# Kernel optimization log

Measured on AMD Instinct MI355X. Metric: run time of the kernel, lower is better.

The kernel has to match this reference:

```python
import jax, jax.numpy as jnp
import numpy as np

DT_MIN, DT_MAX = 0.001, 0.1
CHUNK = 64


def setup_inputs() -> dict:
    key = jax.random.key(0)
    ks = jax.random.split(key, 8)
    b, L, D = 2, 4096, 1024
    d_inner, d_state, nheads, K = 2048, 128, 32, 4
    conv_dim = d_inner + 2 * d_state            # 2304
    d_in_proj = 2 * d_inner + 2 * d_state + nheads  # 4384
    f32 = jnp.float32
    return {
        'x': jax.random.normal(ks[0], (b, L, D), f32),
        'in_proj_w': jax.random.normal(ks[1], (d_in_proj, D), f32) * (D ** -0.5),
        'conv_w': jax.random.normal(ks[2], (conv_dim, K), f32) * 0.3,
        'conv_b': jnp.zeros((conv_dim,), f32),
        'dt_bias': jax.random.normal(ks[3], (nheads,), f32) * 0.5,
        'A_log': jnp.log(jax.random.uniform(ks[4], (nheads,), f32, 1.0, 16.0)),
        'D_skip': jnp.ones((nheads,), f32),
        'norm_w': jnp.ones((d_inner,), f32),
        'out_proj_w': jax.random.normal(ks[5], (D, d_inner), f32) * (d_inner ** -0.5),
        'ln_w': jnp.ones((D,), f32),
        'ln_b': jnp.zeros((D,), f32),
    }


def reference(x, in_proj_w, conv_w, conv_b, dt_bias, A_log, D_skip, norm_w, out_proj_w, ln_w, ln_b):
    b, L, d_model = x.shape
    d_inner = norm_w.shape[0]
    nheads = A_log.shape[0]
    hd = d_inner // nheads                      # headdim = 64
    conv_dim = conv_w.shape[0]
    d_state = (conv_dim - d_inner) // 2
    Q = CHUNK
    c = L // Q

    # ---- Mamba2 in_proj ----
    zxbcdt = jnp.einsum('bld,kd->blk', x, in_proj_w)
    z = zxbcdt[..., :d_inner]                                   # gate
    xBC = zxbcdt[..., d_inner:d_inner + conv_dim]
    dt_raw = zxbcdt[..., d_inner + conv_dim:]                   # (b,L,h)

    # ---- causal depthwise conv1d (kernel 4) + SiLU ----
    K = conv_w.shape[1]
    xp = jnp.pad(xBC, ((0, 0), (K - 1, 0), (0, 0)))
    conv = sum(xp[:, k:k + L, :] * conv_w[:, k] for k in range(K)) + conv_b
    xBC = jax.nn.silu(conv)
    x_ssm = xBC[..., :d_inner]
    Bm = xBC[..., d_inner:d_inner + d_state]                    # (b,L,n)
    Cm = xBC[..., d_inner + d_state:]                           # (b,L,n)

    # ---- bounded dt (sigmoid, per SSMBlock fix) ----
    dt = DT_MIN + (DT_MAX - DT_MIN) * jax.nn.sigmoid(dt_raw + dt_bias)  # (b,L,h)
    A = -jnp.exp(A_log)                                          # (h,)

    # ---- chunked SSD selective scan ----
    xh = x_ssm.reshape(b, c, Q, nheads, hd)
    dtc = dt.reshape(b, c, Q, nheads)
    x_dt = xh * dtc[..., None]
    dA = jnp.einsum('bcqh,h->bhcq', dtc, A)
    Acum = jnp.cumsum(dA, axis=-1)                               # (b,h,c,Q)
    Bc = Bm.reshape(b, c, Q, d_state)
    Cc = Cm.reshape(b, c, Q, d_state)

    # intra-chunk (diagonal blocks)
    seg = Acum[..., :, None] - Acum[..., None, :]                # (b,h,c,Q,Q)
    mask = jnp.tril(jnp.ones((Q, Q), bool))
    Lmat = jnp.exp(jnp.where(mask, seg, -jnp.inf))
    Yd = jnp.einsum('bcqn,bcsn,bhcqs,bcshp->bcqhp', Cc, Bc, Lmat, x_dt)

    # chunk end-states
    decay_states = jnp.exp(Acum[..., -1:] - Acum)                # (b,h,c,Q)
    states = jnp.einsum('bcqn,bhcq,bcqhp->bchpn', Bc, decay_states, x_dt)
    chunk_decay = jnp.exp(Acum[..., -1])                         # (b,h,c)

    def step(carry, inp):
        st, dec = inp
        return dec[..., None, None] * carry + st, carry

    _, prevs = jax.lax.scan(
        step, jnp.zeros((b, nheads, hd, d_state), x.dtype),
        (jnp.moveaxis(states, 1, 0), jnp.moveaxis(chunk_decay, 2, 0)))
    prevs = jnp.moveaxis(prevs, 0, 1)                            # (b,c,h,p,n)

    # inter-chunk contribution
    Yo = jnp.einsum('bcqn,bchpn,bhcq->bcqhp', Cc, prevs, jnp.exp(Acum))

    Y = (Yd + Yo).reshape(b, L, nheads, hd) + D_skip[None, None, :, None] * xh.reshape(b, L, nheads, hd)
    y = Y.reshape(b, L, d_inner)

    # ---- gated RMSNorm + out_proj ----
    y = y * jax.nn.silu(z)
    y = y * jax.lax.rsqrt(jnp.mean(y * y, axis=-1, keepdims=True) + 1e-5) * norm_w
    out = jnp.einsum('bli,di->bld', y, out_proj_w)

    # ---- SSMBlock: LayerNorm + (eval-mode dropout) + residual ----
    mu = jnp.mean(out, axis=-1, keepdims=True)
    var = jnp.mean((out - mu) ** 2, axis=-1, keepdims=True)
    ln = (out - mu) * jax.lax.rsqrt(var + 1e-5) * ln_w + ln_b
    return x + ln
```

## Files before the change

kernel.cpp:

```cpp
#include <hip/hip_runtime.h>
#include <math.h>

#define BSZ     2
#define LEN     4096
#define DMODEL  1024
#define DINNER  2048
#define DSTATE  128
#define NHEADS  32
#define HDIM    64
#define CONVDIM 2304
#define QC      64
#define NCHUNK  64
#define ROWS    (BSZ*LEN)
#define SDIM    (HDIM*DSTATE)
#define PB      136
#define PT      72
#define CGRP    (CONVDIM/8)

typedef __attribute__((ext_vector_type(8))) short short8;
typedef __attribute__((ext_vector_type(4))) float f32x4;

__device__ __forceinline__ float silu_(float x){ return x / (1.0f + expf(-x)); }
__device__ __forceinline__ float sigm_(float x){ return 1.0f / (1.0f + expf(-x)); }
__device__ __forceinline__ float bf2f(unsigned short u){
    return __uint_as_float(((unsigned int)u) << 16);
}
__device__ __forceinline__ unsigned short f2bf(float f){
    unsigned int u = __float_as_uint(f);
    u = (u + 0x7fffu + ((u >> 16) & 1u)) >> 16;
    return (unsigned short)u;
}

__device__ __forceinline__ int swzcol(int row, int col) {
    return ((((col >> 3) ^ (row >> 3)) & 7) << 3) | (col & 7);
}
__device__ __forceinline__ int swzblk(int row, int blk) {
    return (((blk ^ (row >> 3)) & 7) << 3);
}

__device__ __forceinline__ void gload16(const void* g, void* l) {
    __builtin_amdgcn_global_load_lds(
        (const __attribute__((address_space(1))) unsigned int*)g,
        (__attribute__((address_space(3))) unsigned int*)l, 16, 0, 0);
}

__device__ __forceinline__ void cast4(const float* __restrict__ src,
                                      unsigned short* __restrict__ dst, int i) {
    const float4 v = *(const float4*)(src + (size_t)i * 4);
    ushort4 o;
    o.x = f2bf(v.x); o.y = f2bf(v.y); o.z = f2bf(v.z); o.w = f2bf(v.w);
    *(ushort4*)(dst + (size_t)i * 4) = o;
}

__global__ __launch_bounds__(256) void cast3(const float* __restrict__ s0, unsigned short* __restrict__ d0, int n0,
                                             const float* __restrict__ s1, unsigned short* __restrict__ d1, int n1,
                                             const float* __restrict__ s2, unsigned short* __restrict__ d2, int n2) {
    int i = blockIdx.x * 256 + threadIdx.x;
    if (i < n0) { cast4(s0, d0, i); return; }
    i -= n0;
    if (i < n1) { cast4(s1, d1, i); return; }
    i -= n1;
    if (i < n2) cast4(s2, d2, i);
}

__device__ __forceinline__ void stage_half(const unsigned short* __restrict__ G,
                                           void* ldsbase, int w, int lane,
                                           size_t rowbase, int lda, int kcol) {
#pragma unroll
    for (int u = 0; u < 2; u++) {
        const int f = w * 128 + u * 64 + lane;
        const int r = f >> 3;
        const int cl = (lane & 7) ^ (lane >> 3);
        gload16(G + rowbase + (size_t)r * lda + kcol + cl * 8,
                (char*)ldsbase + f * 16);
    }
}

#define WAITV(n) asm volatile("s_waitcnt vmcnt(" #n ")" ::: "memory")
#define LGKM0    asm volatile("s_waitcnt lgkmcnt(0)" ::: "memory")
#define BARRIER  do { asm volatile("" ::: "memory"); \
                      __builtin_amdgcn_s_barrier();  \
                      asm volatile("" ::: "memory"); } while (0)

#define READ_A(dst, buf, half)                                                \
    _Pragma("unroll")                                                         \
    for (int fr = 0; fr < 4; fr++) {                                          \
        const int r_ = (w & 1) * 64 + fr * 16 + l16;                          \
        _Pragma("unroll")                                                     \
        for (int s = 0; s < 2; s++)                                           \
            dst[fr][s] = *(const short8*)((const char*)&lds[buf][0][half][0]  \
                + r_ * 128 + (((s * 4 + quad) ^ rx7) << 4));                  \
    }
#define READ_B(dst, buf, half)                                                \
    _Pragma("unroll")                                                         \
    for (int fc = 0; fc < 2; fc++) {                                          \
        const int r_ = (w >> 1) * 32 + fc * 16 + l16;                         \
        _Pragma("unroll")                                                     \
        for (int s = 0; s < 2; s++)                                           \
            dst[fc][s] = *(const short8*)((const char*)&lds[buf][1][half][0]  \
                + r_ * 128 + (((s * 4 + quad) ^ rx7) << 4));                  \
    }
#define MFMA16(g, af, bfv)                                                    \
    __builtin_amdgcn_s_setprio(1);                                            \
    _Pragma("unroll")                                                         \
    for (int s = 0; s < 2; s++)                                               \
        _Pragma("unroll")                                                     \
        for (int fr = 0; fr < 4; fr++)                                        \
            _Pragma("unroll")                                                 \
            for (int fc = 0; fc < 2; fc++)                                    \
                acc[g][fr][fc] = __builtin_amdgcn_mfma_f32_16x16x32_bf16(     \
                    af[fr][s], bfv[fc][s], acc[g][fr][fc], 0, 0, 0);          \
    __builtin_amdgcn_s_setprio(0);

template<bool BF16OUT>
__global__ __launch_bounds__(512, 2) void gemm8p(const unsigned short* __restrict__ A,
                                                 const unsigned short* __restrict__ B,
                                                 void* __restrict__ C0,
                                                 void* __restrict__ C1,
                                                 int N, int Kfull, int Ks,
                                                 int gx, int nwg1) {
    __shared__ unsigned short lds[2][2][2][8192];
    const int tid = threadIdx.x;
    const int w = tid >> 6, lane = tid & 63;
    const int quad = lane >> 4, l16 = lane & 15;
    const int rx7 = l16 & 7;

    const int nwg = gridDim.x;
    const int id = blockIdx.x;
    const int q8 = nwg >> 3, r8 = nwg & 7;
    const int xcd = id & 7, idx = id >> 3;
    const int wg = (xcd < r8 ? xcd * (q8 + 1) : r8 * (q8 + 1) + (xcd - r8) * q8) + idx;
    const int sid = wg / nwg1;
    const int wgl = wg % nwg1;
    const int m0 = (wgl / gx) * 256, n0 = (wgl % gx) * 256;
    const int kbase = sid * Ks;
    void* Cout = sid ? C1 : C0;

    const size_t a0r = (size_t)m0 * Kfull;
    const size_t a1r = (size_t)(m0 + 128) * Kfull;
    const size_t b0r = (size_t)n0 * Kfull;
    const size_t b1r = (size_t)(n0 + 128) * Kfull;

    f32x4 acc[4][4][2];
#pragma unroll
    for (int g = 0; g < 4; g++)
#pragma unroll
        for (int i = 0; i < 4; i++)
#pragma unroll
            for (int j = 0; j < 2; j++) acc[g][i][j] = (f32x4){0.f, 0.f, 0.f, 0.f};

    const int NT = Ks >> 6;
    stage_half(A, &lds[0][0][0][0], w, lane, a0r, Kfull, kbase);
    stage_half(B, &lds[0][1][0][0], w, lane, b0r, Kfull, kbase);
    stage_half(A, &lds[0][0][1][0], w, lane, a1r, Kfull, kbase);
    stage_half(B, &lds[0][1][1][0], w, lane, b1r, Kfull, kbase);
    stage_half(A, &lds[1][0][0][0], w, lane, a0r, Kfull, kbase + 64);
    stage_half(B, &lds[1][1][0][0], w, lane, b0r, Kfull, kbase + 64);
    stage_half(A, &lds[1][0][1][0], w, lane, a1r, Kfull, kbase + 64);
    WAITV(6); BARRIER;

    short8 af0[4][2], af1[4][2], bf0[2][2], bf1[2][2];
    for (int p = 0; p < (NT >> 1) - 1; p++) {
        const int kb1 = kbase + (2 * p + 1) * 64;
        const int ka2 = kbase + (2 * p + 2) * 64;
        const int kb2 = kbase + (2 * p + 3) * 64;
        READ_A(af0, 0, 0); READ_B(bf0, 0, 0);
        stage_half(B, &lds[1][1][1][0], w, lane, b1r, Kfull, kb1);
        BARRIER; MFMA16(0, af0, bf0); LGKM0; BARRIER;
        READ_A(af1, 0, 1);
        stage_half(A, &lds[0][0][0][0], w, lane, a0r, Kfull, ka2);
        BARRIER; MFMA16(1, af1, bf0); LGKM0; BARRIER;
        READ_B(bf1, 0, 1);
        stage_half(B, &lds[0][1][0][0], w, lane, b0r, Kfull, ka2);
        BARRIER; MFMA16(2, af0, bf1); LGKM0; BARRIER;
        stage_half(A, &lds[0][0][1][0], w, lane, a1r, Kfull, ka2);
        WAITV(6); BARRIER; MFMA16(3, af1, bf1); LGKM0; BARRIER;
        READ_A(af0, 1, 0); READ_B(bf0, 1, 0);
        stage_half(B, &lds[0][1][1][0], w, lane, b1r, Kfull, ka2);
        BARRIER; MFMA16(0, af0, bf0); LGKM0; BARRIER;
        READ_A(af1, 1, 1);
        stage_half(A, &lds[1][0][0][0], w, lane, a0r, Kfull, kb2);
        BARRIER; MFMA16(1, af1, bf0); LGKM0; BARRIER;
        READ_B(bf1, 1, 1);
        stage_half(B, &lds[1][1][0][0], w, lane, b0r, Kfull, kb2);
        BARRIER; MFMA16(2, af0, bf1); LGKM0; BARRIER;
        stage_half(A, &lds[1][0][1][0], w, lane, a1r, Kfull, kb2);
        WAITV(6); BARRIER; MFMA16(3, af1, bf1); LGKM0; BARRIER;
    }
    READ_A(af0, 0, 0); READ_B(bf0, 0, 0);
    stage_half(B, &lds[1][1][1][0], w, lane, b1r, Kfull, kbase + (NT - 1) * 64);
    MFMA16(0, af0, bf0);
    READ_A(af1, 0, 1);
    MFMA16(1, af1, bf0);
    READ_B(bf1, 0, 1);
    MFMA16(2, af0, bf1);
    MFMA16(3, af1, bf1);
    WAITV(0); LGKM0; BARRIER;
    READ_A(af0, 1, 0); READ_B(bf0, 1, 0);
    MFMA16(0, af0, bf0);
    READ_A(af1, 1, 1);
    MFMA16(1, af1, bf0);
    READ_B(bf1, 1, 1);
    MFMA16(2, af0, bf1);
    MFMA16(3, af1, bf1);

#pragma unroll
    for (int g = 0; g < 4; g++) {
        const int qm = g & 1, qn = g >> 1;
        const int mb = m0 + qm * 128 + (w & 1) * 64;
        const int nb2 = n0 + qn * 128 + (w >> 1) * 32;
#pragma unroll
        for (int fr = 0; fr < 4; fr++)
#pragma unroll
            for (int fc = 0; fc < 2; fc++) {
                const int n = nb2 + fc * 16 + l16;
#pragma unroll
                for (int rr = 0; rr < 4; rr++) {
                    const int m = mb + fr * 16 + quad * 4 + rr;
                    if (BF16OUT)
                        ((unsigned short*)Cout)[(size_t)m * N + n] = f2bf(acc[g][fr][fc][rr]);
                    else
                        ((float*)Cout)[(size_t)m * N + n] = acc[g][fr][fc][rr];
                }
            }
    }
}

__global__ __launch_bounds__(256) void dtproj_mfma(const unsigned short* __restrict__ A,
                                                   const unsigned short* __restrict__ W,
                                                   const float* __restrict__ bias,
                                                   float* __restrict__ dtb,
                                                   int K) {
    __shared__ unsigned short As[4][2][32 * 32];
    __shared__ unsigned short Ws[4][2][32 * 32];
    __shared__ float red[4][32][32];
    const int tid = threadIdx.x;
    const int w = tid >> 6, lane = tid & 63;
    const int quad = lane >> 4, l16 = lane & 15;
    const int m0 = blockIdx.x * 32;
    const int kbeg = w * (1024 / 4);

    f32x4 acc[2][2];
#pragma unroll
    for (int i = 0; i < 2; i++)
#pragma unroll
        for (int j = 0; j < 2; j++) acc[i][j] = (f32x4){0.f, 0.f, 0.f, 0.f};

#define DTSTAGE(buf, kt)                                                      \
    _Pragma("unroll")                                                         \
    for (int u = 0; u < 2; u++) {                                             \
        const int f = u * 64 + lane;                                          \
        const int row = f >> 2, ke = (f & 3) * 8;                             \
        gload16(A + (size_t)(m0 + row) * K + (kt) + ke,                       \
                (char*)&As[w][buf][0] + f * 16);                              \
        gload16(W + (size_t)row * K + (kt) + ke,                              \
                (char*)&Ws[w][buf][0] + f * 16);                              \
    }

    DTSTAGE(0, kbeg);
    int buf = 0;
    for (int it = 0; it < 8; it++) {
        if (it < 7) { DTSTAGE(buf ^ 1, kbeg + (it + 1) * 32); WAITV(4); }
        else        { WAITV(0); }
        short8 af[2], bfr[2];
#pragma unroll
        for (int i = 0; i < 2; i++)
            af[i] = *(const short8*)((const char*)&As[w][buf][0] + (i * 16 + l16) * 64 + quad * 16);
#pragma unroll
        for (int j = 0; j < 2; j++)
            bfr[j] = *(const short8*)((const char*)&Ws[w][buf][0] + (j * 16 + l16) * 64 + quad * 16);
#pragma unroll
        for (int i = 0; i < 2; i++)
#pragma unroll
            for (int j = 0; j < 2; j++)
                acc[i][j] = __builtin_amdgcn_mfma_f32_16x16x32_bf16(
                    af[i], bfr[j], acc[i][j], 0, 0, 0);
        buf ^= 1;
    }
#pragma unroll
    for (int i = 0; i < 2; i++)
#pragma unroll
        for (int j = 0; j < 2; j++)
#pragma unroll
            for (int r = 0; r < 4; r++)
                red[w][i * 16 + quad * 4 + r][j * 16 + l16] = acc[i][j][r];
    __syncthreads();
#pragma unroll
    for (int e = 0; e < 4; e++) {
        const int o = tid + e * 256;
        const int m = o >> 5, hh = o & 31;
        const float v = red[0][m][hh] + red[1][m][hh] + red[2][m][hh] + red[3][m][hh];
        dtb[(size_t)m0 * NHEADS + o] = 0.001f + 0.099f * sigm_(v + bias[hh]);
    }
}

__global__ __launch_bounds__(256) void conv_silu_w(const unsigned short* __restrict__ xbc,
                                                   const float* __restrict__ cw,
                                                   const float* __restrict__ cb,
                                                   unsigned short* __restrict__ xssm,
                                                   unsigned short* __restrict__ Bb,
                                                   unsigned short* __restrict__ Cb) {
    const int idx = blockIdx.x * 256 + threadIdx.x;
    const int g = idx % CGRP;
    const int rowblk = idx / CGRP;
    const long row0 = (long)rowblk * 4;
    const int lbase = (int)(row0 & (LEN - 1));
    const int j0 = g * 8;

    float4 wv[8];
    float cbv[8];
#pragma unroll
    for (int e = 0; e < 8; e++) {
        wv[e] = *(const float4*)(cw + (size_t)(j0 + e) * 4);
        cbv[e] = cb[j0 + e];
    }

    short8 win[4];
    const short8 zero8 = (short8){0, 0, 0, 0, 0, 0, 0, 0};
#pragma unroll
    for (int t = 0; t < 3; t++) {
        const int lr = lbase - 3 + t;
        win[t] = (lr >= 0) ? *(const short8*)(xbc + (row0 - 3 + t) * CONVDIM + j0)
                           : zero8;
    }
#pragma unroll
    for (int i = 0; i < 4; i++) {
        win[3] = *(const short8*)(xbc + (row0 + i) * CONVDIM + j0);
        short8 o;
#pragma unroll
        for (int e = 0; e < 8; e++) {
            float acc = cbv[e];
            acc += bf2f((unsigned short)win[0][e]) * wv[e].x;
            acc += bf2f((unsigned short)win[1][e]) * wv[e].y;
            acc += bf2f((unsigned short)win[2][e]) * wv[e].z;
            acc += bf2f((unsigned short)win[3][e]) * wv[e].w;
            o[e] = (short)f2bf(silu_(acc));
        }
        const long row = row0 + i;
        if (j0 < DINNER)
            *(short8*)(xssm + row * DINNER + j0) = o;
        else if (j0 < DINNER + DSTATE)
            *(short8*)(Bb + row * DSTATE + (j0 - DINNER)) = o;
        else
            *(short8*)(Cb + row * DSTATE + (j0 - DINNER - DSTATE)) = o;
        win[0] = win[1]; win[1] = win[2]; win[2] = win[3];
    }
}

__global__ __launch_bounds__(64) void acum_kernel(const float* __restrict__ dtb,
                                                  const float* __restrict__ A_log,
                                                  float* __restrict__ Acum) {
    const int c = blockIdx.x, h = blockIdx.y, b = blockIdx.z;
    const int q = threadIdx.x;
    const float Av = -expf(A_log[h]);
    float v = dtb[((size_t)b * LEN + c * QC + q) * NHEADS + h] * Av;
#pragma unroll
    for (int off = 1; off < 64; off <<= 1) {
        const float n = __shfl_up(v, off, 64);
        if (q >= off) v += n;
    }
    Acum[(((size_t)b * NHEADS + h) * NCHUNK + c) * QC + q] = v;
}

__global__ __launch_bounds__(256) void chunk_mfma(const unsigned short* __restrict__ xssm,
                                                  const unsigned short* __restrict__ Bb,
                                                  const unsigned short* __restrict__ Cb,
                                                  const float* __restrict__ dtb,
                                                  const float* __restrict__ Acum,
                                                  const float* __restrict__ Dskip,
                                                  unsigned short* __restrict__ Y,
                                                  unsigned short* __restrict__ states) {
    const int c = blockIdx.x, h = blockIdx.y, b = blockIdx.z;
    const int tid = threadIdx.x;
    const int wave = tid >> 6, lane = tid & 63;
    const int quad = lane >> 4, l16 = lane & 15;

    __shared__ __attribute__((aligned(16))) unsigned short Bsh[8704];
    __shared__ __attribute__((aligned(16))) unsigned short Csh[9216];
    __shared__ __attribute__((aligned(16))) unsigned short xTs[4608];
    __shared__ float ac[QC], dts[QC], decs[QC];

    const size_t rowbase = (size_t)b * LEN + c * QC;
    if (tid < QC) {
        ac[tid]  = Acum[(((size_t)b * NHEADS + h) * NCHUNK + c) * QC + tid];
        dts[tid] = dtb[(rowbase + tid) * NHEADS + h];
    }
#pragma unroll
    for (int u = 0; u < 4; u++) {
        const int vi = u * 256 + tid;
        const int s = vi >> 4, n0 = (vi & 15) * 8;
        *(short8*)&Bsh[s * PB + n0] = *(const short8*)(Bb + (rowbase + s) * DSTATE + n0);
        *(short8*)&Csh[s * PB + n0] = *(const short8*)(Cb + (rowbase + s) * DSTATE + n0);
    }
#pragma unroll
    for (int u = 0; u < 2; u++) {
        const int vi = u * 256 + tid;
        const int q = vi >> 3, p0 = (vi & 7) * 8;
        const short8 v = *(const short8*)(xssm + (rowbase + q) * DINNER + h * HDIM + p0);
#pragma unroll
        for (int j = 0; j < 8; j++) {
            const int p = p0 + j;
            xTs[p * PT + swzcol(p, q)] = (unsigned short)v[j];
        }
    }
    __syncthreads();
    if (tid < QC) decs[tid] = expf(ac[QC - 1] - ac[tid]) * dts[tid];

    f32x4 S[4];
#pragma unroll
    for (int j = 0; j < 4; j++) S[j] = (f32x4){0.f, 0.f, 0.f, 0.f};
    const int qa = wave * 16 + l16;
#pragma unroll
    for (int ks = 0; ks < 4; ks++) {
        const short8 a = *(const short8*)&Csh[qa * PB + ks * 32 + quad * 8];
#pragma unroll
        for (int j = 0; j < 4; j++) {
            const short8 bb = *(const short8*)&Bsh[(j * 16 + l16) * PB + ks * 32 + quad * 8];
            S[j] = __builtin_amdgcn_mfma_f32_16x16x32_bf16(a, bb, S[j], 0, 0, 0);
        }
    }
    unsigned short slv[4][4];
#pragma unroll
    for (int j = 0; j < 4; j++)
#pragma unroll
        for (int r = 0; r < 4; r++) {
            const int q = wave * 16 + quad * 4 + r, s = j * 16 + l16;
            const float v = (s <= q) ? S[j][r] * expf(ac[q] - ac[s]) * dts[s] : 0.f;
            slv[j][r] = f2bf(v);
        }
    __syncthreads();

    {
        const int sin = lane & 7;
        const int ng  = lane >> 3;
#pragma unroll
        for (int so = 0; so < 2; so++) {
            const int s = (wave * 2 + so) * 8 + sin;
            const float d = decs[s];
            const int cbk = s >> 3;
#pragma unroll
            for (int nh = 0; nh < 2; nh++) {
                const int noct = ng + 8 * nh;
                const int colphys = (((cbk ^ noct) & 7) << 3) | (s & 7);
#pragma unroll
                for (int j = 0; j < 8; j++) {
                    const int n = noct * 8 + ((j + sin) & 7);
                    Csh[n * PT + colphys] = f2bf(bf2f(Bsh[s * PB + n]) * d);
                }
            }
        }
    }
    __syncthreads();

#pragma unroll
    for (int j = 0; j < 4; j++)
#pragma unroll
        for (int r = 0; r < 4; r++) {
            const int row = wave * 16 + quad * 4 + r;
            const int col = j * 16 + l16;
            Bsh[row * PT + swzcol(row, col)] = slv[j][r];
        }
    __syncthreads();

    f32x4 yd[4];
#pragma unroll
    for (int j = 0; j < 4; j++) yd[j] = (f32x4){0.f, 0.f, 0.f, 0.f};
#pragma unroll
    for (int ks = 0; ks < 2; ks++) {
        const int blk = ks * 4 + quad;
        const short8 a = *(const short8*)&Bsh[qa * PT + swzblk(qa, blk)];
#pragma unroll
        for (int j = 0; j < 4; j++) {
            const int row = j * 16 + l16;
            const short8 xb = *(const short8*)&xTs[row * PT + swzblk(row, blk)];
            yd[j] = __builtin_amdgcn_mfma_f32_16x16x32_bf16(a, xb, yd[j], 0, 0, 0);
        }
    }
    const float Dh = Dskip[h];
#pragma unroll
    for (int j = 0; j < 4; j++)
#pragma unroll
        for (int r = 0; r < 4; r++) {
            const int q = wave * 16 + quad * 4 + r, p = j * 16 + l16;
            const float v = yd[j][r] + Dh * bf2f(xTs[p * PT + swzcol(p, q)]);
            Y[(rowbase + q) * DINNER + h * HDIM + p] = f2bf(v);
        }

    f32x4 st[8];
#pragma unroll
    for (int j = 0; j < 8; j++) st[j] = (f32x4){0.f, 0.f, 0.f, 0.f};
#pragma unroll
    for (int ks = 0; ks < 2; ks++) {
        const int blk = ks * 4 + quad;
        const short8 a = *(const short8*)&xTs[qa * PT + swzblk(qa, blk)];
#pragma unroll
        for (int j = 0; j < 8; j++) {
            const int row = j * 16 + l16;
            const short8 bb = *(const short8*)&Csh[row * PT + swzblk(row, blk)];
            st[j] = __builtin_amdgcn_mfma_f32_16x16x32_bf16(a, bb, st[j], 0, 0, 0);
        }
    }
    const size_t sbase = (((size_t)b * NHEADS + h) * NCHUNK + c) * SDIM;
#pragma unroll
    for (int j = 0; j < 8; j++)
#pragma unroll
        for (int r = 0; r < 4; r++) {
            const int p = wave * 16 + quad * 4 + r, n = j * 16 + l16;
            states[sbase + (size_t)p * DSTATE + n] = f2bf(st[j][r]);
        }
}

__global__ __launch_bounds__(256) void scan_kernel(unsigned short* __restrict__ states,
                                                   const float* __restrict__ Acum) {
    __shared__ float dec[NCHUNK];
    const int bh = blockIdx.y;
    const int pn = blockIdx.x * 256 + threadIdx.x;
    if (threadIdx.x < NCHUNK)
        dec[threadIdx.x] = expf(Acum[((size_t)bh * NCHUNK + threadIdx.x) * QC + (QC - 1)]);
    __syncthreads();
    float carry = 0.f;
    const size_t base = (size_t)bh * NCHUNK * SDIM + pn;
    for (int c = 0; c < NCHUNK; c++) {
        const size_t idx = base + (size_t)c * SDIM;
        const float s = bf2f(states[idx]);
        states[idx] = f2bf(carry);
        carry = dec[c] * carry + s;
    }
}

__global__ __launch_bounds__(256) void yo_mfma(const unsigned short* __restrict__ Cb,
                                               const unsigned short* __restrict__ prevs,
                                               const float* __restrict__ Acum,
                                               unsigned short* __restrict__ Y) {
    const int c = blockIdx.x, h = blockIdx.y, b = blockIdx.z;
    const int tid = threadIdx.x;
    const int wave = tid >> 6, lane = tid & 63;
    const int quad = lane >> 4, l16 = lane & 15;
    __shared__ __attribute__((aligned(16))) unsigned short Csh[8704];
    __shared__ __attribute__((aligned(16))) unsigned short Psh[8704];
    __shared__ float eq[QC];
    const size_t rowbase = (size_t)b * LEN + c * QC;
    const size_t pbase = (((size_t)b * NHEADS + h) * NCHUNK + c) * SDIM;
    if (tid < QC)
        eq[tid] = expf(Acum[(((size_t)b * NHEADS + h) * NCHUNK + c) * QC + tid]);
#pragma unroll
    for (int u = 0; u < 4; u++) {
        const int vi = u * 256 + tid;
        const int r = vi >> 4, n0 = (vi & 15) * 8;
        *(short8*)&Csh[r * PB + n0] = *(const short8*)(Cb + (rowbase + r) * DSTATE + n0);
        *(short8*)&Psh[r * PB + n0] = *(const short8*)(prevs + pbase + (size_t)r * DSTATE + n0);
    }
    __syncthreads();

    f32x4 acc[4];
#pragma unroll
    for (int j = 0; j < 4; j++) acc[j] = (f32x4){0.f, 0.f, 0.f, 0.f};
    const int qa = wave * 16 + l16;
#pragma unroll
    for (int ks = 0; ks < 4; ks++) {
        const short8 a = *(const short8*)&Csh[qa * PB + ks * 32 + quad * 8];
#pragma unroll
        for (int j = 0; j < 4; j++) {
            const short8 bb = *(const short8*)&Psh[(j * 16 + l16) * PB + ks * 32 + quad * 8];
            acc[j] = __builtin_amdgcn_mfma_f32_16x16x32_bf16(a, bb, acc[j], 0, 0, 0);
        }
    }
#pragma unroll
    for (int j = 0; j < 4; j++)
#pragma unroll
        for (int r = 0; r < 4; r++) {
            const int q = wave * 16 + quad * 4 + r, p = j * 16 + l16;
            const size_t off = (rowbase + q) * DINNER + h * HDIM + p;
            Y[off] = f2bf(bf2f(Y[off]) + eq[q] * acc[j][r]);
        }
}

__global__ __launch_bounds__(256) void gate_rms(const unsigned short* __restrict__ Y,
                                                const unsigned short* __restrict__ zbf,
                                                const float* __restrict__ nw,
                                                unsigned short* __restrict__ ybf) {
    const int r = blockIdx.x, tid = threadIdx.x;
    float4 yv[2];
    float ss = 0.f;
#pragma unroll
    for (int u = 0; u < 2; u++) {
        const int col = u * 1024 + tid * 4;
        const ushort4 y4 = *(const ushort4*)(Y + (size_t)r * DINNER + col);
        const ushort4 z4 = *(const ushort4*)(zbf + (size_t)r * DINNER + col);
        float4 y;
        y.x = bf2f(y4.x) * silu_(bf2f(z4.x)); y.y = bf2f(y4.y) * silu_(bf2f(z4.y));
        y.z = bf2f(y4.z) * silu_(bf2f(z4.z)); y.w = bf2f(y4.w) * silu_(bf2f(z4.w));
        yv[u] = y;
        ss += y.x * y.x + y.y * y.y + y.z * y.z + y.w * y.w;
    }
#pragma unroll
    for (int off = 32; off; off >>= 1) ss += __shfl_xor(ss, off, 64);
    __shared__ float red[4];
    if ((tid & 63) == 0) red[tid >> 6] = ss;
    __syncthreads();
    ss = red[0] + red[1] + red[2] + red[3];
    const float scale = rsqrtf(ss / (float)DINNER + 1e-5f);
#pragma unroll
    for (int u = 0; u < 2; u++) {
        const int col = u * 1024 + tid * 4;
        const float4 w4 = *(const float4*)(nw + col);
        ushort4 o;
        o.x = f2bf(yv[u].x * scale * w4.x); o.y = f2bf(yv[u].y * scale * w4.y);
        o.z = f2bf(yv[u].z * scale * w4.z); o.w = f2bf(yv[u].w * scale * w4.w);
        *(ushort4*)(ybf + (size_t)r * DINNER + col) = o;
    }
}

__global__ __launch_bounds__(256) void ln_res(const float* __restrict__ outb,
                                              const float* __restrict__ part,
                                              const float* __restrict__ x,
                                              const float* __restrict__ lw,
                                              const float* __restrict__ lb,
                                              float* __restrict__ out) {
    const int r = blockIdx.x, tid = threadIdx.x;
    const int col = tid * 4;
    float4 v = *(const float4*)(outb + (size_t)r * DMODEL + col);
    const float4 pv = *(const float4*)(part + (size_t)r * DMODEL + col);
    v.x += pv.x; v.y += pv.y; v.z += pv.z; v.w += pv.w;
    float s = v.x + v.y + v.z + v.w;
    float s2 = v.x * v.x + v.y * v.y + v.z * v.z + v.w * v.w;
#pragma unroll
    for (int off = 32; off; off >>= 1) {
        s += __shfl_xor(s, off, 64);
        s2 += __shfl_xor(s2, off, 64);
    }
    __shared__ float rs[4], rs2[4];
    if ((tid & 63) == 0) { rs[tid >> 6] = s; rs2[tid >> 6] = s2; }
    __syncthreads();
    s = rs[0] + rs[1] + rs[2] + rs[3];
    s2 = rs2[0] + rs2[1] + rs2[2] + rs2[3];
    const float mu = s / (float)DMODEL;
    const float var = s2 / (float)DMODEL - mu * mu;
    const float inv = rsqrtf(var + 1e-5f);
    const float4 xw = *(const float4*)(x + (size_t)r * DMODEL + col);
    const float4 w4 = *(const float4*)(lw + col);
    const float4 b4 = *(const float4*)(lb + col);
    float4 o;
    o.x = xw.x + (v.x - mu) * inv * w4.x + b4.x;
    o.y = xw.y + (v.y - mu) * inv * w4.y + b4.y;
    o.z = xw.z + (v.z - mu) * inv * w4.z + b4.z;
    o.w = xw.w + (v.w - mu) * inv * w4.w + b4.w;
    *(float4*)(out + (size_t)r * DMODEL + col) = o;
}

extern "C" void kernel_launch(void* const* d_in, const int* in_sizes, int n_in,
                              void* d_out, int out_size, void* d_ws, size_t ws_size,
                              hipStream_t stream) {
    const float* x          = (const float*)d_in[0];
    const float* in_proj_w  = (const float*)d_in[1];
    const float* conv_w     = (const float*)d_in[2];
    const float* conv_b     = (const float*)d_in[3];
    const float* dt_bias    = (const float*)d_in[4];
    const float* A_log      = (const float*)d_in[5];
    const float* D_skip     = (const float*)d_in[6];
    const float* norm_w     = (const float*)d_in[7];
    const float* out_proj_w = (const float*)d_in[8];
    const float* ln_w       = (const float*)d_in[9];
    const float* ln_b       = (const float*)d_in[10];
    float* out = (float*)d_out;
    float* ws = (float*)d_ws;

    size_t off = 0;
    unsigned short* zbf     = (unsigned short*)(ws + off); off += (size_t)ROWS * DINNER / 2;
    unsigned short* xssm_bf = (unsigned short*)(ws + off); off += (size_t)ROWS * DINNER / 2;
    unsigned short* uni     = (unsigned short*)(ws + off); off += (size_t)ROWS * CONVDIM / 2;
    unsigned short* Bb_bf   = (unsigned short*)(ws + off); off += (size_t)ROWS * DSTATE / 2;
    unsigned short* Cb_bf   = (unsigned short*)(ws + off); off += (size_t)ROWS * DSTATE / 2;
    float* dtb   = ws + off; off += (size_t)ROWS * NHEADS;
    float* Acum  = ws + off; off += (size_t)BSZ * NHEADS * NCHUNK * QC;
    unsigned short* x_bf  = (unsigned short*)(ws + off); off += (size_t)ROWS * DMODEL / 2;
    unsigned short* wi_bf = (unsigned short*)(ws + off); off += (size_t)4384 * DMODEL / 2;
    unsigned short* wo_bf = (unsigned short*)(ws + off); off += (size_t)DMODEL * DINNER / 2;
    unsigned short* states = (unsigned short*)(ws + off); off += (size_t)BSZ * NHEADS * NCHUNK * SDIM / 2;
    float* part = ws + off; off += (size_t)ROWS * DMODEL;
    const size_t need_bytes = off * sizeof(float);
    if (ws_size < need_bytes) return;

    unsigned short* xbc_bf = uni;
    unsigned short* Ybf    = uni;
    unsigned short* ybf    = xssm_bf;

    {
        const int n0 = ROWS * DMODEL / 4, n1 = 4384 * DMODEL / 4, n2 = DMODEL * DINNER / 4;
        cast3<<<(n0 + n1 + n2 + 255) / 256, 256, 0, stream>>>(
            x, x_bf, n0, in_proj_w, wi_bf, n1, out_proj_w, wo_bf, n2);
    }

    gemm8p<true><<<(ROWS / 256) * (DINNER / 256), 512, 0, stream>>>(
        x_bf, wi_bf, zbf, nullptr, DINNER, DMODEL, DMODEL,
        DINNER / 256, (ROWS / 256) * (DINNER / 256));
    gemm8p<true><<<(ROWS / 256) * (CONVDIM / 256), 512, 0, stream>>>(
        x_bf, wi_bf + (size_t)DINNER * DMODEL, xbc_bf, nullptr, CONVDIM, DMODEL, DMODEL,
        CONVDIM / 256, (ROWS / 256) * (CONVDIM / 256));
    dtproj_mfma<<<ROWS / 32, 256, 0, stream>>>(
        x_bf, wi_bf + (size_t)(DINNER + CONVDIM) * DMODEL, dt_bias, dtb, DMODEL);

    conv_silu_w<<<(ROWS / 4) * CGRP / 256, 256, 0, stream>>>(
        xbc_bf, conv_w, conv_b, xssm_bf, Bb_bf, Cb_bf);
    acum_kernel<<<dim3(NCHUNK, NHEADS, BSZ), 64, 0, stream>>>(dtb, A_log, Acum);
    chunk_mfma<<<dim3(NCHUNK, NHEADS, BSZ), 256, 0, stream>>>(
        xssm_bf, Bb_bf, Cb_bf, dtb, Acum, D_skip, Ybf, states);
    scan_kernel<<<dim3(SDIM / 256, BSZ * NHEADS), 256, 0, stream>>>(states, Acum);
    yo_mfma<<<dim3(NCHUNK, NHEADS, BSZ), 256, 0, stream>>>(Cb_bf, states, Acum, Ybf);
    gate_rms<<<ROWS, 256, 0, stream>>>(Ybf, zbf, norm_w, ybf);

    gemm8p<false><<<2 * (ROWS / 256) * (DMODEL / 256), 512, 0, stream>>>(
        ybf, wo_bf, out, part, DMODEL, DINNER, DINNER / 2,
        DMODEL / 256, (ROWS / 256) * (DMODEL / 256));
    ln_res<<<ROWS, 256, 0, stream>>>(out, part, x, ln_w, ln_b, out);
}
```

Before: 402.7 us.

## Merge in_proj GEMMs into one persistent kernel with split-K tail and fold Acum scan

Result: slower. 453.3 us (+12.6%).

```diff
diff --git a/kernel.cpp b/kernel.cpp
--- a/kernel.cpp
+++ b/kernel.cpp
@@ -113,33 +113,21 @@
     __builtin_amdgcn_s_setprio(0);
 
 template<bool BF16OUT>
-__global__ __launch_bounds__(512, 2) void gemm8p(const unsigned short* __restrict__ A,
-                                                 const unsigned short* __restrict__ B,
-                                                 void* __restrict__ C0,
-                                                 void* __restrict__ C1,
-                                                 int N, int Kfull, int Ks,
-                                                 int gx, int nwg1) {
-    __shared__ unsigned short lds[2][2][2][8192];
+__device__ __forceinline__ void tile256(unsigned short (&lds)[2][2][2][8192],
+                                        const unsigned short* __restrict__ Apan,
+                                        const unsigned short* __restrict__ Bpan,
+                                        void* __restrict__ Cout,
+                                        int N, int m0, int n0,
+                                        int Kfull, int kbase, int Ks) {
     const int tid = threadIdx.x;
     const int w = tid >> 6, lane = tid & 63;
     const int quad = lane >> 4, l16 = lane & 15;
     const int rx7 = l16 & 7;
 
-    const int nwg = gridDim.x;
-    const int id = blockIdx.x;
-    const int q8 = nwg >> 3, r8 = nwg & 7;
-    const int xcd = id & 7, idx = id >> 3;
-    const int wg = (xcd < r8 ? xcd * (q8 + 1) : r8 * (q8 + 1) + (xcd - r8) * q8) + idx;
-    const int sid = wg / nwg1;
-    const int wgl = wg % nwg1;
-    const int m0 = (wgl / gx) * 256, n0 = (wgl % gx) * 256;
-    const int kbase = sid * Ks;
-    void* Cout = sid ? C1 : C0;
-
-    const size_t a0r = (size_t)m0 * Kfull;
-    const size_t a1r = (size_t)(m0 + 128) * Kfull;
-    const size_t b0r = (size_t)n0 * Kfull;
-    const size_t b1r = (size_t)(n0 + 128) * Kfull;
+    const size_t a0r = 0;
+    const size_t a1r = (size_t)128 * Kfull;
+    const size_t b0r = 0;
+    const size_t b1r = (size_t)128 * Kfull;
 
     f32x4 acc[4][4][2];
 #pragma unroll
@@ -150,13 +138,14 @@
             for (int j = 0; j < 2; j++) acc[g][i][j] = (f32x4){0.f, 0.f, 0.f, 0.f};
 
     const int NT = Ks >> 6;
-    stage_half(A, &lds[0][0][0][0], w, lane, a0r, Kfull, kbase);
-    stage_half(B, &lds[0][1][0][0], w, lane, b0r, Kfull, kbase);
-    stage_half(A, &lds[0][0][1][0], w, lane, a1r, Kfull, kbase);
-    stage_half(B, &lds[0][1][1][0], w, lane, b1r, Kfull, kbase);
-    stage_half(A, &lds[1][0][0][0], w, lane, a0r, Kfull, kbase + 64);
-    stage_half(B, &lds[1][1][0][0], w, lane, b0r, Kfull, kbase + 64);
-    stage_half(A, &lds[1][0][1][0], w, lane, a1r, Kfull, kbase + 64);
+    BARRIER;
+    stage_half(Apan, &lds[0][0][0][0], w, lane, a0r, Kfull, kbase);
+    stage_half(Bpan, &lds[0][1][0][0], w, lane, b0r, Kfull, kbase);
+    stage_half(Apan, &lds[0][0][1][0], w, lane, a1r, Kfull, kbase);
+    stage_half(Bpan, &lds[0][1][1][0], w, lane, b1r, Kfull, kbase);
+    stage_half(Apan, &lds[1][0][0][0], w, lane, a0r, Kfull, kbase + 64);
+    stage_half(Bpan, &lds[1][1][0][0], w, lane, b0r, Kfull, kbase + 64);
+    stage_half(Apan, &lds[1][0][1][0], w, lane, a1r, Kfull, kbase + 64);
     WAITV(6); BARRIER;
 
     short8 af0[4][2], af1[4][2], bf0[2][2], bf1[2][2];
@@ -165,30 +154,30 @@
         const int ka2 = kbase + (2 * p + 2) * 64;
         const int kb2 = kbase + (2 * p + 3) * 64;
         READ_A(af0, 0, 0); READ_B(bf0, 0, 0);
-        stage_half(B, &lds[1][1][1][0], w, lane, b1r, Kfull, kb1);
+        stage_half(Bpan, &lds[1][1][1][0], w, lane, b1r, Kfull, kb1);
         BARRIER; MFMA16(0, af0, bf0); LGKM0; BARRIER;
         READ_A(af1, 0, 1);
-        stage_half(A, &lds[0][0][0][0], w, lane, a0r, Kfull, ka2);
+        stage_half(Apan, &lds[0][0][0][0], w, lane, a0r, Kfull, ka2);
         BARRIER; MFMA16(1, af1, bf0); LGKM0; BARRIER;
         READ_B(bf1, 0, 1);
-        stage_half(B, &lds[0][1][0][0], w, lane, b0r, Kfull, ka2);
+        stage_half(Bpan, &lds[0][1][0][0], w, lane, b0r, Kfull, ka2);
         BARRIER; MFMA16(2, af0, bf1); LGKM0; BARRIER;
-        stage_half(A, &lds[0][0][1][0], w, lane, a1r, Kfull, ka2);
+        stage_half(Apan, &lds[0][0][1][0], w, lane, a1r, Kfull, ka2);
         WAITV(6); BARRIER; MFMA16(3, af1, bf1); LGKM0; BARRIER;
         READ_A(af0, 1, 0); READ_B(bf0, 1, 0);
-        stage_half(B, &lds[0][1][1][0], w, lane, b1r, Kfull, ka2);
+        stage_half(Bpan, &lds[0][1][1][0], w, lane, b1r, Kfull, ka2);
         BARRIER; MFMA16(0, af0, bf0); LGKM0; BARRIER;
         READ_A(af1, 1, 1);
-        stage_half(A, &lds[1][0][0][0], w, lane, a0r, Kfull, kb2);
+        stage_half(Apan, &lds[1][0][0][0], w, lane, a0r, Kfull, kb2);
         BARRIER; MFMA16(1, af1, bf0); LGKM0; BARRIER;
         READ_B(bf1, 1, 1);
-        stage_half(B, &lds[1][1][0][0], w, lane, b0r, Kfull, kb2);
+        stage_half(Bpan, &lds[1][1][0][0], w, lane, b0r, Kfull, kb2);
         BARRIER; MFMA16(2, af0, bf1); LGKM0; BARRIER;
-        stage_half(A, &lds[1][0][1][0], w, lane, a1r, Kfull, kb2);
+        stage_half(Apan, &lds[1][0][1][0], w, lane, a1r, Kfull, kb2);
         WAITV(6); BARRIER; MFMA16(3, af1, bf1); LGKM0; BARRIER;
     }
     READ_A(af0, 0, 0); READ_B(bf0, 0, 0);
-    stage_half(B, &lds[1][1][1][0], w, lane, b1r, Kfull, kbase + (NT - 1) * 64);
+    stage_half(Bpan, &lds[1][1][1][0], w, lane, b1r, Kfull, kbase + (NT - 1) * 64);
     MFMA16(0, af0, bf0);
     READ_A(af1, 0, 1);
     MFMA16(1, af1, bf0);
@@ -226,6 +215,73 @@
     }
 }
 
+template<bool BF16OUT>
+__global__ __launch_bounds__(512, 2) void gemm8p(const unsigned short* __restrict__ A,
+                                                 const unsigned short* __restrict__ B,
+                                                 void* __restrict__ C0,
+                                                 void* __restrict__ C1,
+                                                 int N, int Kfull, int Ks,
+                                                 int gx, int nwg1) {
+    __shared__ unsigned short lds[2][2][2][8192];
+    const int nwg = gridDim.x;
+    const int id = blockIdx.x;
+    const int q8 = nwg >> 3, r8 = nwg & 7;
+    const int xcd = id & 7, idx = id >> 3;
+    const int wg = (xcd < r8 ? xcd * (q8 + 1) : r8 * (q8 + 1) + (xcd - r8) * q8) + idx;
+    const int sid = wg / nwg1;
+    const int wgl = wg % nwg1;
+    const int m0 = (wgl / gx) * 256, n0 = (wgl % gx) * 256;
+    tile256<BF16OUT>(lds, A + (size_t)m0 * Kfull, B + (size_t)n0 * Kfull,
+                     sid ? C1 : C0, N, m0, n0, Kfull, sid * Ks, Ks);
+}
+
+__global__ __launch_bounds__(512, 2) void inproj_mfma(const unsigned short* __restrict__ x_bf,
+                                                      const unsigned short* __restrict__ wi,
+                                                      unsigned short* __restrict__ zbf,
+                                                      unsigned short* __restrict__ xbc,
+                                                      float* __restrict__ part0,
+                                                      float* __restrict__ part1) {
+    __shared__ unsigned short lds[2][2][2][8192];
+    const int id = blockIdx.x;
+    const int wg = (id & 7) * 32 + (id >> 3);
+#pragma unroll
+    for (int ti = 0; ti < 2; ti++) {
+        const int t = wg + ti * 256;
+        const int nt = t >> 5, mt = t & 31;
+        const int m0 = mt * 256;
+        const unsigned short* Apan = x_bf + (size_t)m0 * DMODEL;
+        const unsigned short* Bpan = wi + (size_t)nt * 256 * DMODEL;
+        if (nt < 8)
+            tile256<true>(lds, Apan, Bpan, zbf, DINNER, m0, nt * 256,
+                          DMODEL, 0, DMODEL);
+        else
+            tile256<true>(lds, Apan, Bpan, xbc, CONVDIM, m0, (nt - 8) * 256,
+                          DMODEL, 0, DMODEL);
+    }
+    if ((wg & 3) == 0) {
+        const int hi = wg >> 2;
+        const int mt = hi >> 1, kh = hi & 1;
+        const int m0 = mt * 256;
+        tile256<false>(lds, x_bf + (size_t)m0 * DMODEL,
+                       wi + (size_t)4096 * DMODEL,
+                       kh ? (void*)part1 : (void*)part0, 256, m0, 0,
+                       DMODEL, kh * 512, 512);
+    }
+}
+
+__global__ __launch_bounds__(256) void xbc_fix(const float* __restrict__ p0,
+                                               const float* __restrict__ p1,
+                                               unsigned short* __restrict__ xbc) {
+    const int i = (blockIdx.x * 256 + threadIdx.x) * 4;
+    const int m = i >> 8, n = i & 255;
+    const float4 a = *(const float4*)(p0 + i);
+    const float4 b = *(const float4*)(p1 + i);
+    ushort4 o;
+    o.x = f2bf(a.x + b.x); o.y = f2bf(a.y + b.y);
+    o.z = f2bf(a.z + b.z); o.w = f2bf(a.w + b.w);
+    *(ushort4*)(xbc + (size_t)m * CONVDIM + 2048 + n) = o;
+}
+
 __global__ __launch_bounds__(256) void dtproj_mfma(const unsigned short* __restrict__ A,
                                                    const unsigned short* __restrict__ W,
                                                    const float* __restrict__ bias,
@@ -347,26 +403,12 @@
     }
 }
 
-__global__ __launch_bounds__(64) void acum_kernel(const float* __restrict__ dtb,
-                                                  const float* __restrict__ A_log,
-                                                  float* __restrict__ Acum) {
-    const int c = blockIdx.x, h = blockIdx.y, b = blockIdx.z;
-    const int q = threadIdx.x;
-    const float Av = -expf(A_log[h]);
-    float v = dtb[((size_t)b * LEN + c * QC + q) * NHEADS + h] * Av;
-#pragma unroll
-    for (int off = 1; off < 64; off <<= 1) {
-        const float n = __shfl_up(v, off, 64);
-        if (q >= off) v += n;
-    }
-    Acum[(((size_t)b * NHEADS + h) * NCHUNK + c) * QC + q] = v;
-}
-
 __global__ __launch_bounds__(256) void chunk_mfma(const unsigned short* __restrict__ xssm,
                                                   const unsigned short* __restrict__ Bb,
                                                   const unsigned short* __restrict__ Cb,
                                                   const float* __restrict__ dtb,
-                                                  const float* __restrict__ Acum,
+                                                  const float* __restrict__ A_log,
+                                                  float* __restrict__ Acum,
                                                   const float* __restrict__ Dskip,
                                                   unsigned short* __restrict__ Y,
                                                   unsigned short* __restrict__ states) {
@@ -382,8 +424,16 @@
 
     const size_t rowbase = (size_t)b * LEN + c * QC;
     if (tid < QC) {
-        ac[tid]  = Acum[(((size_t)b * NHEADS + h) * NCHUNK + c) * QC + tid];
-        dts[tid] = dtb[(rowbase + tid) * NHEADS + h];
+        const float d = dtb[(rowbase + tid) * NHEADS + h];
+        dts[tid] = d;
+        float v = d * (-expf(A_log[h]));
+#pragma unroll
+        for (int off2 = 1; off2 < 64; off2 <<= 1) {
+            const float nv = __shfl_up(v, off2, 64);
+            if (tid >= off2) v += nv;
+        }
+        ac[tid] = v;
+        Acum[(((size_t)b * NHEADS + h) * NCHUNK + c) * QC + tid] = v;
     }
 #pragma unroll
     for (int u = 0; u < 4; u++) {
@@ -684,6 +734,8 @@
     unsigned short* xbc_bf = uni;
     unsigned short* Ybf    = uni;
     unsigned short* ybf    = xssm_bf;
+    float* ip_p0 = part;
+    float* ip_p1 = part + (size_t)ROWS * 256;
 
     {
         const int n0 = ROWS * DMODEL / 4, n1 = 4384 * DMODEL / 4, n2 = DMODEL * DINNER / 4;
@@ -691,20 +743,15 @@
             x, x_bf, n0, in_proj_w, wi_bf, n1, out_proj_w, wo_bf, n2);
     }
 
-    gemm8p<true><<<(ROWS / 256) * (DINNER / 256), 512, 0, stream>>>(
-        x_bf, wi_bf, zbf, nullptr, DINNER, DMODEL, DMODEL,
-        DINNER / 256, (ROWS / 256) * (DINNER / 256));
-    gemm8p<true><<<(ROWS / 256) * (CONVDIM / 256), 512, 0, stream>>>(
-        x_bf, wi_bf + (size_t)DINNER * DMODEL, xbc_bf, nullptr, CONVDIM, DMODEL, DMODEL,
-        CONVDIM / 256, (ROWS / 256) * (CONVDIM / 256));
+    inproj_mfma<<<256, 512, 0, stream>>>(x_bf, wi_bf, zbf, xbc_bf, ip_p0, ip_p1);
+    xbc_fix<<<ROWS * 256 / 1024, 256, 0, stream>>>(ip_p0, ip_p1, xbc_bf);
     dtproj_mfma<<<ROWS / 32, 256, 0, stream>>>(
         x_bf, wi_bf + (size_t)(DINNER + CONVDIM) * DMODEL, dt_bias, dtb, DMODEL);
 
     conv_silu_w<<<(ROWS / 4) * CGRP / 256, 256, 0, stream>>>(
         xbc_bf, conv_w, conv_b, xssm_bf, Bb_bf, Cb_bf);
-    acum_kernel<<<dim3(NCHUNK, NHEADS, BSZ), 64, 0, stream>>>(dtb, A_log, Acum);
     chunk_mfma<<<dim3(NCHUNK, NHEADS, BSZ), 256, 0, stream>>>(
-        xssm_bf, Bb_bf, Cb_bf, dtb, Acum, D_skip, Ybf, states);
+        xssm_bf, Bb_bf, Cb_bf, dtb, A_log, Acum, D_skip, Ybf, states);
     scan_kernel<<<dim3(SDIM / 256, BSZ * NHEADS), 256, 0, stream>>>(states, Acum);
     yo_mfma<<<dim3(NCHUNK, NHEADS, BSZ), 256, 0, stream>>>(Cb_bf, states, Acum, Ybf);
     gate_rms<<<ROWS, 256, 0, stream>>>(Ybf, zbf, norm_w, ybf);
```
